# Kernel optimization log

Hardware: AMD Instinct MI355X
Metric: run time of the kernel (lower is better)

## Reference

```python
import jax, jax.numpy as jnp
import numpy as np

B = 4096
FEATURE_SIZE = 64 * 64 * 10  # 40960 (HalfKP)
H1, H2, H3 = 256, 32, 32
NNZ = 30  # ~pieces on board per side


def _onehot_multi(key, batch, dim, nnz):
    # Build sparse feature vectors: nnz ones scattered per row (matches HalfKP usage).
    idx = jax.random.randint(key, (batch, nnz), 0, dim)
    x = jnp.zeros((batch, dim), dtype=jnp.float32)
    rows = jnp.arange(batch)[:, None]
    return x.at[rows, idx].set(1.0)


def setup_inputs() -> dict:
    key = jax.random.key(0)
    kw, kb, k1, k2, k3, k4, k5 = jax.random.split(key, 7)
    # xavier_uniform with gain=0.5: bound = 0.5 * sqrt(6/(fan_in+fan_out))
    def xavier(k, out_f, in_f):
        bound = 0.5 * np.sqrt(6.0 / (in_f + out_f))
        return jax.random.uniform(k, (out_f, in_f), jnp.float32, -bound, bound)
    return {
        "white_features": _onehot_multi(kw, B, FEATURE_SIZE, NNZ),
        "black_features": _onehot_multi(kb, B, FEATURE_SIZE, NNZ),
        "ft_w": xavier(k1, H1, FEATURE_SIZE),
        "ft_b": jnp.zeros((H1,), jnp.float32),
        "fc1_w": xavier(k2, H2, 2 * H1),
        "fc1_b": jnp.zeros((H2,), jnp.float32),
        "fc2_w": xavier(k3, H3, H2),
        "fc2_b": jnp.zeros((H3,), jnp.float32),
        "fc3_w": xavier(k4, 1, H3),
        "fc3_b": jnp.zeros((1,), jnp.float32),
    }


def _crelu(x):
    return jnp.clip(x, 0.0, 1.0)


def reference(white_features, black_features, ft_w, ft_b, fc1_w, fc1_b,
              fc2_w, fc2_b, fc3_w, fc3_b):
    # feature transform (dense equivalent of sparse gather-sum)
    w = _crelu(white_features @ ft_w.T + ft_b)  # [B, 256]
    b = _crelu(black_features @ ft_w.T + ft_b)  # [B, 256]
    x = jnp.concatenate([w, b], axis=1)          # [B, 512]
    x = _crelu(x @ fc1_w.T + fc1_b)              # [B, 32]
    x = _crelu(x @ fc2_w.T + fc2_b)              # [B, 32]
    return x @ fc3_w.T + fc3_b                   # [B, 1]
```

## Files before the change

### kernel.cpp

```cpp
#include <hip/hip_runtime.h>
#include <hip/hip_bf16.h>

#define FEAT 40960
#define NH1  256
#define MAXNZ 128

typedef float vfloat4 __attribute__((ext_vector_type(4)));

__global__ __launch_bounds__(256) void transpose_ftw(const float* __restrict__ ft_w,
                                                     float* __restrict__ ft_wt) {
    __shared__ float tile[32][33];
    const int i0 = blockIdx.x * 32;
    const int h0 = blockIdx.y * 32;
    const int tx = threadIdx.x;
    const int ty = threadIdx.y;
#pragma unroll
    for (int j = 0; j < 4; ++j) {
        tile[ty + j * 8][tx] = ft_w[(size_t)(h0 + ty + j * 8) * FEAT + i0 + tx];
    }
    __syncthreads();
#pragma unroll
    for (int j = 0; j < 4; ++j) {
        ft_wt[(size_t)(i0 + ty + j * 8) * NH1 + h0 + tx] = tile[tx][ty + j * 8];
    }
}

__global__ __launch_bounds__(256) void nnue_fused(
    const float* __restrict__ wf,
    const float* __restrict__ bfeat,
    const float* __restrict__ ft_wt,
    const float* __restrict__ ft_b,
    const float* __restrict__ fc1_w,
    const float* __restrict__ fc1_b,
    const float* __restrict__ fc2_w,
    const float* __restrict__ fc2_b,
    const float* __restrict__ fc3_w,
    const float* __restrict__ fc3_b,
    float* __restrict__ out)
{
    __shared__ int   idxw[MAXNZ], idxb[MAXNZ];
    __shared__ float valw[MAXNZ], valb[MAXNZ];
    __shared__ int   cntw, cntb;
    __shared__ float xsh[512];
    __shared__ float red[256];
    __shared__ float h1[32], h2[32];

    const int tid = threadIdx.x;
    const int b   = blockIdx.x;

    if (tid == 0) { cntw = 0; cntb = 0; }
    __syncthreads();

    const vfloat4* wf4 = (const vfloat4*)(wf    + (size_t)b * FEAT);
    const vfloat4* bf4 = (const vfloat4*)(bfeat + (size_t)b * FEAT);
    constexpr int ITERS = FEAT / 4 / 256;
#pragma unroll 4
    for (int it = 0; it < ITERS; ++it) {
        const int k4 = it * 256 + tid;
        const vfloat4 vw = wf4[k4];
        const vfloat4 vb = bf4[k4];
        const int base = k4 * 4;
        const bool anyw = (vw.x != 0.f) | (vw.y != 0.f) | (vw.z != 0.f) | (vw.w != 0.f);
        const bool anyb = (vb.x != 0.f) | (vb.y != 0.f) | (vb.z != 0.f) | (vb.w != 0.f);
        if (__any(anyw)) {
            if (vw.x != 0.f) { int p = atomicAdd(&cntw, 1); if (p < MAXNZ) { idxw[p] = base + 0; valw[p] = vw.x; } }
            if (vw.y != 0.f) { int p = atomicAdd(&cntw, 1); if (p < MAXNZ) { idxw[p] = base + 1; valw[p] = vw.y; } }
            if (vw.z != 0.f) { int p = atomicAdd(&cntw, 1); if (p < MAXNZ) { idxw[p] = base + 2; valw[p] = vw.z; } }
            if (vw.w != 0.f) { int p = atomicAdd(&cntw, 1); if (p < MAXNZ) { idxw[p] = base + 3; valw[p] = vw.w; } }
        }
        if (__any(anyb)) {
            if (vb.x != 0.f) { int p = atomicAdd(&cntb, 1); if (p < MAXNZ) { idxb[p] = base + 0; valb[p] = vb.x; } }
            if (vb.y != 0.f) { int p = atomicAdd(&cntb, 1); if (p < MAXNZ) { idxb[p] = base + 1; valb[p] = vb.y; } }
            if (vb.z != 0.f) { int p = atomicAdd(&cntb, 1); if (p < MAXNZ) { idxb[p] = base + 2; valb[p] = vb.z; } }
            if (vb.w != 0.f) { int p = atomicAdd(&cntb, 1); if (p < MAXNZ) { idxb[p] = base + 3; valb[p] = vb.w; } }
        }
    }
    __syncthreads();
    const int nw = min(cntw, MAXNZ);
    const int nb = min(cntb, MAXNZ);

    float aw0 = ft_b[tid], aw1 = 0.f;
    float ab0 = aw0,       ab1 = 0.f;
    const int nmin = min(nw, nb);
    int j = 0;
    for (; j + 2 <= nmin; j += 2) {
        const float w0 = ft_wt[(size_t)idxw[j]     * NH1 + tid];
        const float w1 = ft_wt[(size_t)idxw[j + 1] * NH1 + tid];
        const float b0 = ft_wt[(size_t)idxb[j]     * NH1 + tid];
        const float b1 = ft_wt[(size_t)idxb[j + 1] * NH1 + tid];
        aw0 += valw[j] * w0;  aw1 += valw[j + 1] * w1;
        ab0 += valb[j] * b0;  ab1 += valb[j + 1] * b1;
    }
    for (int jw = j; jw < nw; ++jw) aw0 += valw[jw] * ft_wt[(size_t)idxw[jw] * NH1 + tid];
    for (int jb = j; jb < nb; ++jb) ab0 += valb[jb] * ft_wt[(size_t)idxb[jb] * NH1 + tid];

    xsh[tid]       = fminf(fmaxf(aw0 + aw1, 0.f), 1.f);
    xsh[256 + tid] = fminf(fmaxf(ab0 + ab1, 0.f), 1.f);
    __syncthreads();

    {
        const int o = tid & 31, part = tid >> 5;
        const float* wrow = fc1_w + o * 512 + part * 64;
        const float* xp   = xsh + part * 64;
        float s = 0.f;
#pragma unroll
        for (int k = 0; k < 64; ++k) s += wrow[k] * xp[k];
        red[tid] = s;
    }
    __syncthreads();
    if (tid < 32) {
        float s = fc1_b[tid];
#pragma unroll
        for (int p = 0; p < 8; ++p) s += red[tid + p * 32];
        h1[tid] = fminf(fmaxf(s, 0.f), 1.f);
    }
    __syncthreads();

    if (tid < 32) {
        float s = fc2_b[tid];
#pragma unroll
        for (int k = 0; k < 32; ++k) s += fc2_w[tid * 32 + k] * h1[k];
        h2[tid] = fminf(fmaxf(s, 0.f), 1.f);
    }
    __syncthreads();

    if (tid == 0) {
        float s = fc3_b[0];
#pragma unroll
        for (int k = 0; k < 32; ++k) s += fc3_w[k] * h2[k];
        out[b] = s;
    }
}

extern "C" void kernel_launch(void* const* d_in, const int* in_sizes, int n_in,
                              void* d_out, int out_size, void* d_ws, size_t ws_size,
                              hipStream_t stream) {
    const float* wf    = (const float*)d_in[0];
    const float* bfeat = (const float*)d_in[1];
    const float* ft_w  = (const float*)d_in[2];
    const float* ft_b  = (const float*)d_in[3];
    const float* fc1_w = (const float*)d_in[4];
    const float* fc1_b = (const float*)d_in[5];
    const float* fc2_w = (const float*)d_in[6];
    const float* fc2_b = (const float*)d_in[7];
    const float* fc3_w = (const float*)d_in[8];
    const float* fc3_b = (const float*)d_in[9];
    float* out = (float*)d_out;

    const int B = in_sizes[0] / FEAT;
    float* ft_wt = (float*)d_ws;

    {
        dim3 blk(32, 8);
        dim3 grd(FEAT / 32, NH1 / 32);
        transpose_ftw<<<grd, blk, 0, stream>>>(ft_w, ft_wt);
    }
    nnue_fused<<<B, 256, 0, stream>>>(wf, bfeat, ft_wt,
                                      ft_b, fc1_w, fc1_b, fc2_w, fc2_b,
                                      fc3_w, fc3_b, out);
}
```

Measured before the change: 1.282 ms.

## Split sparse scan into separate compaction kernel with nontemporal loads

Splits the fused kernel into two launches. The first scans each white and black feature row in its own block (2B blocks) with nontemporal loads and writes the compacted indices and values to workspace. The second reads those lists, does the gather and runs the MLP. This doubles the parallelism of the bandwidth-bound scan and keeps the streamed input from evicting the transposed weights from cache. The cost is an extra launch and a small workspace round trip.

```diff
diff --git a/kernel.cpp b/kernel.cpp
--- a/kernel.cpp
+++ b/kernel.cpp
@@ -25,9 +25,54 @@
     }
 }
 
-__global__ __launch_bounds__(256) void nnue_fused(
+__global__ __launch_bounds__(256) void scan_compact(
     const float* __restrict__ wf,
     const float* __restrict__ bfeat,
+    int B,
+    int*   __restrict__ cnts,
+    int*   __restrict__ lidx,
+    float* __restrict__ lval)
+{
+    __shared__ int   idx[MAXNZ];
+    __shared__ float val[MAXNZ];
+    __shared__ int   cnt;
+
+    const int tid = threadIdx.x;
+    const int r   = blockIdx.x;
+    const float* src = (r < B) ? (wf + (size_t)r * FEAT)
+                               : (bfeat + (size_t)(r - B) * FEAT);
+    if (tid == 0) cnt = 0;
+    __syncthreads();
+
+    const vfloat4* s4 = (const vfloat4*)src;
+    constexpr int ITERS = FEAT / 4 / 256;
+#pragma unroll 4
+    for (int it = 0; it < ITERS; ++it) {
+        const int k4 = it * 256 + tid;
+        const vfloat4 v = __builtin_nontemporal_load(s4 + k4);
+        const int base = k4 * 4;
+        const bool any = (v.x != 0.f) | (v.y != 0.f) | (v.z != 0.f) | (v.w != 0.f);
+        if (__any(any)) {
+            if (v.x != 0.f) { int p = atomicAdd(&cnt, 1); if (p < MAXNZ) { idx[p] = base + 0; val[p] = v.x; } }
+            if (v.y != 0.f) { int p = atomicAdd(&cnt, 1); if (p < MAXNZ) { idx[p] = base + 1; val[p] = v.y; } }
+            if (v.z != 0.f) { int p = atomicAdd(&cnt, 1); if (p < MAXNZ) { idx[p] = base + 2; val[p] = v.z; } }
+            if (v.w != 0.f) { int p = atomicAdd(&cnt, 1); if (p < MAXNZ) { idx[p] = base + 3; val[p] = v.w; } }
+        }
+    }
+    __syncthreads();
+    const int n = min(cnt, MAXNZ);
+    if (tid == 0) cnts[r] = n;
+    if (tid < n) {
+        lidx[(size_t)r * MAXNZ + tid] = idx[tid];
+        lval[(size_t)r * MAXNZ + tid] = val[tid];
+    }
+}
+
+__global__ __launch_bounds__(256) void gather_mlp(
+    const int*   __restrict__ cnts,
+    const int*   __restrict__ lidx,
+    const float* __restrict__ lval,
+    int B,
     const float* __restrict__ ft_wt,
     const float* __restrict__ ft_b,
     const float* __restrict__ fc1_w,
@@ -40,7 +85,6 @@
 {
     __shared__ int   idxw[MAXNZ], idxb[MAXNZ];
     __shared__ float valw[MAXNZ], valb[MAXNZ];
-    __shared__ int   cntw, cntb;
     __shared__ float xsh[512];
     __shared__ float red[256];
     __shared__ float h1[32], h2[32];
@@ -48,36 +92,13 @@
     const int tid = threadIdx.x;
     const int b   = blockIdx.x;
 
-    if (tid == 0) { cntw = 0; cntb = 0; }
+    const int nw = cnts[b];
+    const int nb = cnts[B + b];
+    if (tid < nw) { idxw[tid] = lidx[(size_t)b * MAXNZ + tid];
+                    valw[tid] = lval[(size_t)b * MAXNZ + tid]; }
+    if (tid < nb) { idxb[tid] = lidx[(size_t)(B + b) * MAXNZ + tid];
+                    valb[tid] = lval[(size_t)(B + b) * MAXNZ + tid]; }
     __syncthreads();
-
-    const vfloat4* wf4 = (const vfloat4*)(wf    + (size_t)b * FEAT);
-    const vfloat4* bf4 = (const vfloat4*)(bfeat + (size_t)b * FEAT);
-    constexpr int ITERS = FEAT / 4 / 256;
-#pragma unroll 4
-    for (int it = 0; it < ITERS; ++it) {
-        const int k4 = it * 256 + tid;
-        const vfloat4 vw = wf4[k4];
-        const vfloat4 vb = bf4[k4];
-        const int base = k4 * 4;
-        const bool anyw = (vw.x != 0.f) | (vw.y != 0.f) | (vw.z != 0.f) | (vw.w != 0.f);
-        const bool anyb = (vb.x != 0.f) | (vb.y != 0.f) | (vb.z != 0.f) | (vb.w != 0.f);
-        if (__any(anyw)) {
-            if (vw.x != 0.f) { int p = atomicAdd(&cntw, 1); if (p < MAXNZ) { idxw[p] = base + 0; valw[p] = vw.x; } }
-            if (vw.y != 0.f) { int p = atomicAdd(&cntw, 1); if (p < MAXNZ) { idxw[p] = base + 1; valw[p] = vw.y; } }
-            if (vw.z != 0.f) { int p = atomicAdd(&cntw, 1); if (p < MAXNZ) { idxw[p] = base + 2; valw[p] = vw.z; } }
-            if (vw.w != 0.f) { int p = atomicAdd(&cntw, 1); if (p < MAXNZ) { idxw[p] = base + 3; valw[p] = vw.w; } }
-        }
-        if (__any(anyb)) {
-            if (vb.x != 0.f) { int p = atomicAdd(&cntb, 1); if (p < MAXNZ) { idxb[p] = base + 0; valb[p] = vb.x; } }
-            if (vb.y != 0.f) { int p = atomicAdd(&cntb, 1); if (p < MAXNZ) { idxb[p] = base + 1; valb[p] = vb.y; } }
-            if (vb.z != 0.f) { int p = atomicAdd(&cntb, 1); if (p < MAXNZ) { idxb[p] = base + 2; valb[p] = vb.z; } }
-            if (vb.w != 0.f) { int p = atomicAdd(&cntb, 1); if (p < MAXNZ) { idxb[p] = base + 3; valb[p] = vb.w; } }
-        }
-    }
-    __syncthreads();
-    const int nw = min(cntw, MAXNZ);
-    const int nb = min(cntb, MAXNZ);
 
     float aw0 = ft_b[tid], aw1 = 0.f;
     float ab0 = aw0,       ab1 = 0.f;
@@ -148,14 +169,20 @@
     float* out = (float*)d_out;
 
     const int B = in_sizes[0] / FEAT;
-    float* ft_wt = (float*)d_ws;
+
+    char* ws = (char*)d_ws;
+    float* ft_wt = (float*)ws;
+    int*   cnts  = (int*)  (ws + (48u << 20));
+    int*   lidx  = (int*)  (ws + (52u << 20));
+    float* lval  = (float*)(ws + (60u << 20));
 
     {
         dim3 blk(32, 8);
         dim3 grd(FEAT / 32, NH1 / 32);
         transpose_ftw<<<grd, blk, 0, stream>>>(ft_w, ft_wt);
     }
-    nnue_fused<<<B, 256, 0, stream>>>(wf, bfeat, ft_wt,
+    scan_compact<<<2 * B, 256, 0, stream>>>(wf, bfeat, B, cnts, lidx, lval);
+    gather_mlp<<<B, 256, 0, stream>>>(cnts, lidx, lval, B, ft_wt,
                                       ft_b, fc1_w, fc1_b, fc2_w, fc2_b,
                                       fc3_w, fc3_b, out);
 }
```

Result: no change. 1.261 ms (-1.6%).

## Stream sparse feature rows into LDS with double-buffered async global_load_lds

Applied to the files above, without the earlier changes.

The dense feature-row scan now gives each wave one half of either the white or the black row, instead of having every thread read both rows. Each wave issues 16-byte global_load_lds transfers straight into a per-wave double-buffered LDS stage, and uses explicit vmcnt waits to overlap the next chunk's load with scanning the current one. Nonzero detection switches to an integer bitwise test on the staged words. The aim is more memory traffic in flight on this bandwidth-bound scan. The cost is 32KB of extra LDS per block, which may lower occupancy, plus reliance on hand-written waitcnt ordering.

```diff
diff --git a/kernel.cpp b/kernel.cpp
--- a/kernel.cpp
+++ b/kernel.cpp
@@ -5,7 +5,8 @@
 #define NH1  256
 #define MAXNZ 128
 
-typedef float vfloat4 __attribute__((ext_vector_type(4)));
+typedef float        vfloat4 __attribute__((ext_vector_type(4)));
+typedef unsigned int vuint4  __attribute__((ext_vector_type(4)));
 
 __global__ __launch_bounds__(256) void transpose_ftw(const float* __restrict__ ft_w,
                                                      float* __restrict__ ft_wt) {
@@ -38,6 +39,7 @@
     const float* __restrict__ fc3_b,
     float* __restrict__ out)
 {
+    __shared__ vuint4 stage[4][2][256];
     __shared__ int   idxw[MAXNZ], idxb[MAXNZ];
     __shared__ float valw[MAXNZ], valb[MAXNZ];
     __shared__ int   cntw, cntb;
@@ -45,34 +47,58 @@
     __shared__ float red[256];
     __shared__ float h1[32], h2[32];
 
-    const int tid = threadIdx.x;
-    const int b   = blockIdx.x;
+    const int tid  = threadIdx.x;
+    const int b    = blockIdx.x;
+    const int w    = tid >> 6;
+    const int lane = tid & 63;
 
     if (tid == 0) { cntw = 0; cntb = 0; }
     __syncthreads();
 
-    const vfloat4* wf4 = (const vfloat4*)(wf    + (size_t)b * FEAT);
-    const vfloat4* bf4 = (const vfloat4*)(bfeat + (size_t)b * FEAT);
-    constexpr int ITERS = FEAT / 4 / 256;
-#pragma unroll 4
-    for (int it = 0; it < ITERS; ++it) {
-        const int k4 = it * 256 + tid;
-        const vfloat4 vw = wf4[k4];
-        const vfloat4 vb = bf4[k4];
-        const int base = k4 * 4;
-        const bool anyw = (vw.x != 0.f) | (vw.y != 0.f) | (vw.z != 0.f) | (vw.w != 0.f);
-        const bool anyb = (vb.x != 0.f) | (vb.y != 0.f) | (vb.z != 0.f) | (vb.w != 0.f);
-        if (__any(anyw)) {
-            if (vw.x != 0.f) { int p = atomicAdd(&cntw, 1); if (p < MAXNZ) { idxw[p] = base + 0; valw[p] = vw.x; } }
-            if (vw.y != 0.f) { int p = atomicAdd(&cntw, 1); if (p < MAXNZ) { idxw[p] = base + 1; valw[p] = vw.y; } }
-            if (vw.z != 0.f) { int p = atomicAdd(&cntw, 1); if (p < MAXNZ) { idxw[p] = base + 2; valw[p] = vw.z; } }
-            if (vw.w != 0.f) { int p = atomicAdd(&cntw, 1); if (p < MAXNZ) { idxw[p] = base + 3; valw[p] = vw.w; } }
+    const bool  isWhite = (w < 2);
+    const char* src = (const char*)((isWhite ? wf : bfeat) + (size_t)b * FEAT)
+                      + (w & 1) * (FEAT / 2) * 4;
+    const int   ebase0 = (w & 1) * (FEAT / 2);
+    int*   cp = isWhite ? &cntw : &cntb;
+    int*   ip = isWhite ? idxw  : idxb;
+    float* vp = isWhite ? valw  : valb;
+
+    constexpr int STEPS = (FEAT / 2) * 4 / 4096;
+
+#pragma unroll
+    for (int u = 0; u < 4; ++u) {
+        __builtin_amdgcn_global_load_lds(
+            (const __attribute__((address_space(1))) void*)(src + u * 1024 + lane * 16),
+            (__attribute__((address_space(3))) void*)(&stage[w][0][u * 64]),
+            16, 0, 0);
+    }
+
+    for (int s = 0; s < STEPS; ++s) {
+        const int cur = s & 1;
+        if (s + 1 < STEPS) {
+            const char* nsrc = src + (s + 1) * 4096;
+#pragma unroll
+            for (int u = 0; u < 4; ++u) {
+                __builtin_amdgcn_global_load_lds(
+                    (const __attribute__((address_space(1))) void*)(nsrc + u * 1024 + lane * 16),
+                    (__attribute__((address_space(3))) void*)(&stage[w][cur ^ 1][u * 64]),
+                    16, 0, 0);
+            }
+            asm volatile("s_waitcnt vmcnt(4)" ::: "memory");
+        } else {
+            asm volatile("s_waitcnt vmcnt(0)" ::: "memory");
         }
-        if (__any(anyb)) {
-            if (vb.x != 0.f) { int p = atomicAdd(&cntb, 1); if (p < MAXNZ) { idxb[p] = base + 0; valb[p] = vb.x; } }
-            if (vb.y != 0.f) { int p = atomicAdd(&cntb, 1); if (p < MAXNZ) { idxb[p] = base + 1; valb[p] = vb.y; } }
-            if (vb.z != 0.f) { int p = atomicAdd(&cntb, 1); if (p < MAXNZ) { idxb[p] = base + 2; valb[p] = vb.z; } }
-            if (vb.w != 0.f) { int p = atomicAdd(&cntb, 1); if (p < MAXNZ) { idxb[p] = base + 3; valb[p] = vb.w; } }
+        __builtin_amdgcn_sched_barrier(0);
+#pragma unroll
+        for (int u = 0; u < 4; ++u) {
+            const vuint4 v = stage[w][cur][u * 64 + lane];
+            if (__any((v.x | v.y | v.z | v.w) != 0u)) {
+                const int e = ebase0 + ((s * 4096 + u * 1024 + lane * 16) >> 2);
+                if (v.x) { int p = atomicAdd(cp, 1); if (p < MAXNZ) { ip[p] = e + 0; vp[p] = __uint_as_float(v.x); } }
+                if (v.y) { int p = atomicAdd(cp, 1); if (p < MAXNZ) { ip[p] = e + 1; vp[p] = __uint_as_float(v.y); } }
+                if (v.z) { int p = atomicAdd(cp, 1); if (p < MAXNZ) { ip[p] = e + 2; vp[p] = __uint_as_float(v.z); } }
+                if (v.w) { int p = atomicAdd(cp, 1); if (p < MAXNZ) { ip[p] = e + 3; vp[p] = __uint_as_float(v.w); } }
+            }
         }
     }
     __syncthreads();
```

Measured after the change: 1.273 ms. Within noise of the previous version (-0.7%).
